# Performance work log

Hardware: AMD Instinct MI355X
Metric: run time of the kernel (lower is better)

## Reference

```python
import jax, jax.numpy as jnp
import numpy as np

B, S, D, E, K, NS = 4, 1024, 1024, 8, 2, 2
H = 4 * D
TEMP = 0.1
SCALE = 0.02


def setup_inputs() -> dict:
    key = jax.random.key(0)
    ks = jax.random.split(key, 12)
    f32 = jnp.float32
    return {
        "x": jax.random.normal(ks[0], (B, S, D), f32),
        "Ws1": jax.random.normal(ks[1], (NS, D, H), f32) * SCALE,
        "bs1": jnp.zeros((NS, H), f32),
        "Ws2": jax.random.normal(ks[2], (NS, H, D), f32) * SCALE,
        "bs2": jnp.zeros((NS, D), f32),
        "We1": jax.random.normal(ks[3], (E, D, H), f32) * SCALE,
        "be1": jnp.zeros((E, H), f32),
        "We2": jax.random.normal(ks[4], (E, H, D), f32) * SCALE,
        "be2": jnp.zeros((E, D), f32),
        "Wr": jax.random.normal(ks[5], (D, E), f32) * SCALE,
        "br": jnp.zeros((E,), f32),
        "gumbel": jax.random.gumbel(ks[6], (B, S, E), f32),
    }


def reference(x, Ws1, bs1, Ws2, bs2, We1, be1, We2, be2, Wr, br, gumbel):
    act = jax.nn.gelu
    # shared experts: dense FFN per shared expert, summed over experts
    hs = act(jnp.einsum('bsd,edh->ebsh', x, Ws1) + bs1[:, None, None, :])
    shared_sum = (jnp.einsum('ebsh,ehd->ebsd', hs, Ws2)
                  + bs2[:, None, None, :]).sum(axis=0)  # [B,S,D]
    # routing experts: ALL experts computed densely over all tokens
    he = act(jnp.einsum('bsd,edh->ebsh', x, We1) + be1[:, None, None, :])
    all_experts = jnp.einsum('ebsh,ehd->ebsd', he, We2) + be2[:, None, None, :]  # [E,B,S,D]
    # router + gumbel-softmax top-k selection
    logits = x @ Wr + br                                  # [B,S,E]
    router_probs = jax.nn.softmax((logits + gumbel) / TEMP, axis=-1)
    chosen = jax.lax.top_k(router_probs, K)[1]            # [B,S,K] int
    one_hot = jax.nn.one_hot(chosen, E, dtype=x.dtype)    # [B,S,K,E]
    # unweighted sum of selected experts' outputs (sum over k and experts)
    out = jnp.einsum('bske,ebsd->bsd', one_hot, all_experts)
    return out + shared_sum
```

## Files before the change

kernel.cpp:

```cpp
#include <hip/hip_runtime.h>
#include <cstdint>
#include <cstddef>

#define T_TOK 4096
#define DDIM 1024
#define HDIM 4096
#define NEXP 8
#define NSHARED 2
#define RT_CAP 9216

typedef unsigned short ushort_t;
typedef __attribute__((ext_vector_type(8))) short short8;
typedef __attribute__((ext_vector_type(4))) float f32x4;

__device__ inline ushort_t f2bf(float f) {
  unsigned u = __float_as_uint(f);
  u += 0x7fffu + ((u >> 16) & 1u);
  return (ushort_t)(u >> 16);
}

__device__ inline void async_copy16(const ushort_t* g, ushort_t* l) {
  __builtin_amdgcn_global_load_lds(
      (const __attribute__((address_space(1))) void*)g,
      (__attribute__((address_space(3))) void*)l, 16, 0, 0);
}

__device__ inline float gelu_tanh(float x) {
  float x2 = x * x;
  float t = fmaf(0.07135481627133721f, x2, 1.5957691216057308f);
  float e = __expf(-x * t);
  return x * __builtin_amdgcn_rcpf(1.0f + e);
}

__device__ inline void swizzle_xy(int* bx, int* by) {
  int l = blockIdx.x + gridDim.x * blockIdx.y;
  int g = l >> 8;
  *bx = (l & 7) + (g << 3);
  *by = (l >> 3) & 31;
}

#define PIPE_BOUNDARY()                                     \
  __builtin_amdgcn_sched_barrier(0);                        \
  asm volatile("s_waitcnt vmcnt(4)" ::: "memory");          \
  __builtin_amdgcn_s_barrier();                             \
  asm volatile("" ::: "memory");                            \
  __builtin_amdgcn_sched_barrier(0);

__global__ __launch_bounds__(256) void router_kernel(
    const float* __restrict__ x, const float* __restrict__ Wr,
    const float* __restrict__ br, const float* __restrict__ gum,
    int* __restrict__ choice, int* __restrict__ cnt) {
  int lane = threadIdx.x & 63;
  int wv = blockIdx.x * 4 + (threadIdx.x >> 6);
  if (wv >= T_TOK) return;
  const float* xr = x + (long)wv * DDIM;
  float acc[NEXP] = {0.f, 0.f, 0.f, 0.f, 0.f, 0.f, 0.f, 0.f};
  for (int d = lane; d < DDIM; d += 64) {
    float xv = xr[d];
    const float* w = Wr + d * NEXP;
#pragma unroll
    for (int e = 0; e < NEXP; e++) acc[e] += xv * w[e];
  }
#pragma unroll
  for (int e = 0; e < NEXP; e++) {
    float v = acc[e];
#pragma unroll
    for (int o = 32; o > 0; o >>= 1) v += __shfl_down(v, o);
    acc[e] = v;
  }
  if (lane == 0) {
    float vals[NEXP];
#pragma unroll
    for (int e = 0; e < NEXP; e++) vals[e] = acc[e] + br[e] + gum[(long)wv * NEXP + e];
    int i1 = 0; float b1 = vals[0];
#pragma unroll
    for (int e = 1; e < NEXP; e++) if (vals[e] > b1) { b1 = vals[e]; i1 = e; }
    int i2 = -1; float b2 = -3.4e38f;
#pragma unroll
    for (int e = 0; e < NEXP; e++) if (e != i1 && vals[e] > b2) { b2 = vals[e]; i2 = e; }
    choice[wv] = i1 | (i2 << 4);
    atomicAdd(&cnt[i1], 1);
    atomicAdd(&cnt[i2], 1);
  }
}

__global__ void prefix_kernel(const int* __restrict__ cnt, int* __restrict__ base,
                              int* __restrict__ fill) {
  if (threadIdx.x == 0 && blockIdx.x == 0) {
    int off = 0;
    for (int e = 0; e < NEXP; e++) {
      base[e] = off;
      off += (cnt[e] + 127) & ~127;
      fill[e] = 0;
    }
  }
}

__global__ __launch_bounds__(256) void scatter_kernel(
    const int* __restrict__ choice, const int* __restrict__ base,
    int* __restrict__ fill, int* __restrict__ idx, int* __restrict__ pos) {
  int t = blockIdx.x * 256 + threadIdx.x;
  if (t >= T_TOK) return;
  int c = choice[t];
  int e1 = c & 15, e2 = (c >> 4) & 15;
  int p1 = base[e1] + atomicAdd(&fill[e1], 1);
  idx[p1] = t; pos[2 * t] = p1;
  int p2 = base[e2] + atomicAdd(&fill[e2], 1);
  idx[p2] = t; pos[2 * t + 1] = p2;
}

__global__ __launch_bounds__(256) void cast_x_kernel(
    const float* __restrict__ in, ushort_t* __restrict__ out, int n4) {
  int i = blockIdx.x * 256 + threadIdx.x;
  if (i >= n4) return;
  float4 v = ((const float4*)in)[i];
  ushort4 o = make_ushort4(f2bf(v.x), f2bf(v.y), f2bf(v.z), f2bf(v.w));
  ((ushort4*)out)[i] = o;
}

__global__ __launch_bounds__(256) void transpose_cast10(
    const float* __restrict__ inS, const float* __restrict__ inE,
    ushort_t* __restrict__ out, int R, int C) {
  __shared__ float tile[32][33];
  int z = blockIdx.z;
  const float* in = (z < NSHARED) ? inS + (size_t)z * R * C
                                  : inE + (size_t)(z - NSHARED) * R * C;
  ushort_t* op = out + (size_t)z * R * C;
  int c0 = blockIdx.x * 32, r0 = blockIdx.y * 32;
  int tx = threadIdx.x, ty = threadIdx.y;
#pragma unroll
  for (int k = 0; k < 4; k++)
    tile[ty + 8 * k][tx] = in[(long)(r0 + ty + 8 * k) * C + (c0 + tx)];
  __syncthreads();
#pragma unroll
  for (int k = 0; k < 4; k++)
    op[(long)(c0 + ty + 8 * k) * R + (r0 + tx)] = f2bf(tile[tx][ty + 8 * k]);
}

__global__ __launch_bounds__(256) void gemm1_kernel(
    const ushort_t* __restrict__ xb, const ushort_t* __restrict__ W1t,
    const float* __restrict__ bs1, const float* __restrict__ be1,
    ushort_t* __restrict__ h_sh, ushort_t* __restrict__ h_rt,
    const int* __restrict__ cnt, const int* __restrict__ base,
    const int* __restrict__ idx) {
  __shared__ ushort_t As[3][4096];
  __shared__ ushort_t Bs[3][4096];

  int tid = threadIdx.x;
  int z = blockIdx.z;
  int bx, by; swizzle_xy(&bx, &by);
  int row0 = by * 128, col0 = bx * 128;
  bool sh = (z < NSHARED);

  int e = 0, M = T_TOK, base_e = 0;
  const ushort_t* Bp;
  const float* bias;
  if (sh) {
    Bp = W1t + (size_t)z * HDIM * DDIM;
    bias = bs1 + (size_t)z * HDIM;
  } else {
    e = z - NSHARED; M = cnt[e];
    if (row0 >= M) return;
    base_e = base[e];
    Bp = W1t + (size_t)(NSHARED + e) * HDIM * DDIM;
    bias = be1 + (size_t)e * HDIM;
  }

  int tq = tid & 3, tr = tid >> 2;
  const ushort_t *aP0, *aP1;
  if (sh) {
    aP0 = xb + (size_t)(row0 + tr) * DDIM + tq * 8;
    aP1 = aP0 + (size_t)64 * DDIM;
  } else {
    int s1 = row0 + tr;      if (s1 > M - 1) s1 = M - 1;
    int s2 = row0 + tr + 64; if (s2 > M - 1) s2 = M - 1;
    aP0 = xb + (size_t)idx[base_e + s1] * DDIM + tq * 8;
    aP1 = xb + (size_t)idx[base_e + s2] * DDIM + tq * 8;
  }
  const ushort_t* bP0 = Bp + (size_t)(col0 + tr) * DDIM + tq * 8;
  const ushort_t* bP1 = bP0 + (size_t)64 * DDIM;

  int lane = tid & 63, wv = tid >> 6;
  int wr = wv >> 1, wc = wv & 1;
  int ln = lane & 15, quad = lane >> 4;
  f32x4 acc[4][4] = {};
  const int ofsA = (wr * 64 + ln) * 32 + quad * 8;
  const int ofsB = (wc * 64 + ln) * 32 + quad * 8;

#define G1_STAGE(t, c)                                            \
  {                                                               \
    size_t kk = (size_t)(t) * 32;                                 \
    async_copy16(aP0 + kk, As[c] + tid * 8);                      \
    async_copy16(aP1 + kk, As[c] + tid * 8 + 2048);               \
    async_copy16(bP0 + kk, Bs[c] + tid * 8);                      \
    async_copy16(bP1 + kk, Bs[c] + tid * 8 + 2048);               \
  }

#define G1_COMPUTE(c)                                             \
  {                                                               \
    const ushort_t* aL = As[c] + ofsA;                            \
    const ushort_t* bL = Bs[c] + ofsB;                            \
    short8 af[4], bf[4];                                          \
    _Pragma("unroll") for (int i = 0; i < 4; i++) {               \
      af[i] = *(const short8*)(aL + i * 512);                     \
      bf[i] = *(const short8*)(bL + i * 512);                     \
    }                                                             \
    __builtin_amdgcn_s_setprio(1);                                \
    _Pragma("unroll") for (int i = 0; i < 4; i++)                 \
      _Pragma("unroll") for (int j = 0; j < 4; j++)               \
        acc[i][j] = __builtin_amdgcn_mfma_f32_16x16x32_bf16(      \
            af[i], bf[j], acc[i][j], 0, 0, 0);                    \
    __builtin_amdgcn_s_setprio(0);                                \
  }

  const int NT = DDIM / 32;
  G1_STAGE(0, 0);
  G1_STAGE(1, 1);
  PIPE_BOUNDARY();

  int c0 = 0, c1 = 1, c2 = 2;
  for (int t = 0; t < NT - 2; ++t) {
    G1_STAGE(t + 2, c2);
    G1_COMPUTE(c0);
    PIPE_BOUNDARY();
    int tmp = c0; c0 = c1; c1 = c2; c2 = tmp;
  }
  G1_COMPUTE(c0);
  __syncthreads();
  G1_COMPUTE(c1);

#pragma unroll
  for (int i = 0; i < 4; i++) {
    int rowB = row0 + wr * 64 + i * 16 + quad * 4;
#pragma unroll
    for (int j = 0; j < 4; j++) {
      int col = col0 + wc * 64 + j * 16 + ln;
      float b = bias[col];
#pragma unroll
      for (int r = 0; r < 4; r++) {
        int t = rowB + r;
        float v = gelu_tanh(acc[i][j][r] + b);
        if (sh) {
          h_sh[(size_t)t * (2 * HDIM) + (size_t)z * HDIM + col] = f2bf(v);
        } else if (t < M) {
          h_rt[((size_t)base_e + t) * HDIM + col] = f2bf(v);
        }
      }
    }
  }
#undef G1_STAGE
#undef G1_COMPUTE
}

__global__ __launch_bounds__(256) void gemm2_kernel(
    const ushort_t* __restrict__ h_sh, const ushort_t* __restrict__ h_rt,
    const ushort_t* __restrict__ W2t, float* __restrict__ outShA,
    float* __restrict__ outShB, float* __restrict__ outRt,
    const int* __restrict__ cnt, const int* __restrict__ base) {
  __shared__ ushort_t As[3][4096];
  __shared__ ushort_t Bs[3][4096];

  int tid = threadIdx.x;
  int z = blockIdx.z;
  int bx, by; swizzle_xy(&bx, &by);
  int row0 = by * 128, col0 = bx * 128;
  bool sh = (z < NSHARED);

  int e = 0, M = T_TOK, base_e = 0;
  const ushort_t* Ap;
  long lda;
  const ushort_t* Bp;
  float* outP;
  if (sh) {
    Ap = h_sh + (size_t)z * HDIM;
    lda = 2 * HDIM;
    Bp = W2t + (size_t)z * DDIM * HDIM;
    outP = (z == 0) ? outShA : outShB;
  } else {
    e = z - NSHARED; M = cnt[e];
    if (row0 >= M) return;
    base_e = base[e];
    Ap = h_rt + (size_t)base_e * HDIM;
    lda = HDIM;
    Bp = W2t + (size_t)(NSHARED + e) * DDIM * HDIM;
    outP = outRt + (size_t)base_e * DDIM;
  }

  int tq = tid & 3, tr = tid >> 2;
  const ushort_t* aP0 = Ap + (long)(row0 + tr) * lda + tq * 8;
  const ushort_t* aP1 = aP0 + 64L * lda;
  const ushort_t* bP0 = Bp + (size_t)(col0 + tr) * HDIM + tq * 8;
  const ushort_t* bP1 = bP0 + (size_t)64 * HDIM;

  int lane = tid & 63, wv = tid >> 6;
  int wr = wv >> 1, wc = wv & 1;
  int ln = lane & 15, quad = lane >> 4;
  f32x4 acc[4][4] = {};
  const int ofsA = (wr * 64 + ln) * 32 + quad * 8;
  const int ofsB = (wc * 64 + ln) * 32 + quad * 8;

#define G2_STAGE(t, c)                                            \
  {                                                               \
    size_t kk = (size_t)(t) * 32;                                 \
    async_copy16(aP0 + kk, As[c] + tid * 8);                      \
    async_copy16(aP1 + kk, As[c] + tid * 8 + 2048);               \
    async_copy16(bP0 + kk, Bs[c] + tid * 8);                      \
    async_copy16(bP1 + kk, Bs[c] + tid * 8 + 2048);               \
  }

#define G2_COMPUTE(c)                                             \
  {                                                               \
    const ushort_t* aL = As[c] + ofsA;                            \
    const ushort_t* bL = Bs[c] + ofsB;                            \
    short8 af[4], bf[4];                                          \
    _Pragma("unroll") for (int i = 0; i < 4; i++) {               \
      af[i] = *(const short8*)(aL + i * 512);                     \
      bf[i] = *(const short8*)(bL + i * 512);                     \
    }                                                             \
    __builtin_amdgcn_s_setprio(1);                                \
    _Pragma("unroll") for (int i = 0; i < 4; i++)                 \
      _Pragma("unroll") for (int j = 0; j < 4; j++)               \
        acc[i][j] = __builtin_amdgcn_mfma_f32_16x16x32_bf16(      \
            af[i], bf[j], acc[i][j], 0, 0, 0);                    \
    __builtin_amdgcn_s_setprio(0);                                \
  }

  const int NT = HDIM / 32;
  G2_STAGE(0, 0);
  G2_STAGE(1, 1);
  PIPE_BOUNDARY();

  int c0 = 0, c1 = 1, c2 = 2;
  for (int t = 0; t < NT - 2; ++t) {
    G2_STAGE(t + 2, c2);
    G2_COMPUTE(c0);
    PIPE_BOUNDARY();
    int tmp = c0; c0 = c1; c1 = c2; c2 = tmp;
  }
  G2_COMPUTE(c0);
  __syncthreads();
  G2_COMPUTE(c1);

#pragma unroll
  for (int i = 0; i < 4; i++) {
    int rowB = row0 + wr * 64 + i * 16 + quad * 4;
#pragma unroll
    for (int j = 0; j < 4; j++) {
      int col = col0 + wc * 64 + j * 16 + ln;
#pragma unroll
      for (int r = 0; r < 4; r++) {
        int t = rowB + r;
        if (sh || t < M) outP[(size_t)t * DDIM + col] = acc[i][j][r];
      }
    }
  }
#undef G2_STAGE
#undef G2_COMPUTE
}

__global__ __launch_bounds__(256) void combine_kernel(
    const float* __restrict__ shA, const float* __restrict__ shB,
    const float* __restrict__ rt, const float* __restrict__ bs2,
    const float* __restrict__ be2, const int* __restrict__ choice,
    const int* __restrict__ pos, float* __restrict__ out) {
  int i = blockIdx.x * 256 + threadIdx.x;
  int t = i >> 8;
  int d4 = i & 255;
  int c = choice[t];
  int e1 = c & 15, e2 = (c >> 4) & 15;
  long p1 = (long)pos[2 * t] * 256 + d4;
  long p2 = (long)pos[2 * t + 1] * 256 + d4;
  float4 a = ((const float4*)shA)[i];
  float4 b = ((const float4*)shB)[i];
  float4 r1 = ((const float4*)rt)[p1];
  float4 r2 = ((const float4*)rt)[p2];
  float4 b0 = ((const float4*)bs2)[d4];
  float4 b1 = ((const float4*)bs2)[256 + d4];
  float4 c1 = ((const float4*)be2)[e1 * 256 + d4];
  float4 c2 = ((const float4*)be2)[e2 * 256 + d4];
  float4 o;
  o.x = a.x + b.x + r1.x + r2.x + b0.x + b1.x + c1.x + c2.x;
  o.y = a.y + b.y + r1.y + r2.y + b0.y + b1.y + c1.y + c2.y;
  o.z = a.z + b.z + r1.z + r2.z + b0.z + b1.z + c1.z + c2.z;
  o.w = a.w + b.w + r1.w + r2.w + b0.w + b1.w + c1.w + c2.w;
  ((float4*)out)[i] = o;
}

extern "C" void kernel_launch(void* const* d_in, const int* in_sizes, int n_in,
                              void* d_out, int out_size, void* d_ws,
                              size_t ws_size, hipStream_t stream) {
  const float* x   = (const float*)d_in[0];
  const float* Ws1 = (const float*)d_in[1];
  const float* bs1 = (const float*)d_in[2];
  const float* Ws2 = (const float*)d_in[3];
  const float* bs2 = (const float*)d_in[4];
  const float* We1 = (const float*)d_in[5];
  const float* be1 = (const float*)d_in[6];
  const float* We2 = (const float*)d_in[7];
  const float* be2 = (const float*)d_in[8];
  const float* Wr  = (const float*)d_in[9];
  const float* br  = (const float*)d_in[10];
  const float* gum = (const float*)d_in[11];
  float* out = (float*)d_out;

  char* ws = (char*)d_ws;
  size_t off = 0;
  int* cnt    = (int*)(ws + off); off += 256;
  int* base   = (int*)(ws + off); off += 256;
  int* fill   = (int*)(ws + off); off += 256;
  int* choice = (int*)(ws + off); off += T_TOK * 4;
  int* idx    = (int*)(ws + off); off += RT_CAP * 4;
  int* pos    = (int*)(ws + off); off += T_TOK * 8;
  off = (off + 255) & ~(size_t)255;
  ushort_t* xb   = (ushort_t*)(ws + off); off += (size_t)T_TOK * DDIM * 2;
  ushort_t* W1t  = (ushort_t*)(ws + off); off += (size_t)10 * HDIM * DDIM * 2;
  ushort_t* W2t  = (ushort_t*)(ws + off); off += (size_t)10 * DDIM * HDIM * 2;
  ushort_t* h_sh = (ushort_t*)(ws + off); off += (size_t)T_TOK * 2 * HDIM * 2;
  ushort_t* h_rt = (ushort_t*)(ws + off); off += (size_t)RT_CAP * HDIM * 2;
  float* outShA = (float*)W1t;
  float* outShB = outShA + (size_t)T_TOK * DDIM;
  float* outRt  = outShB + (size_t)T_TOK * DDIM;
  (void)ws_size;

  hipMemsetAsync(cnt, 0, 256, stream);
  router_kernel<<<T_TOK / 4, 256, 0, stream>>>(x, Wr, br, gum, choice, cnt);
  prefix_kernel<<<1, 64, 0, stream>>>(cnt, base, fill);
  scatter_kernel<<<T_TOK / 256, 256, 0, stream>>>(choice, base, fill, idx, pos);
  cast_x_kernel<<<(T_TOK * DDIM / 4 + 255) / 256, 256, 0, stream>>>(
      x, xb, T_TOK * DDIM / 4);

  transpose_cast10<<<dim3(HDIM / 32, DDIM / 32, 10), dim3(32, 8), 0, stream>>>(
      Ws1, We1, W1t, DDIM, HDIM);
  transpose_cast10<<<dim3(DDIM / 32, HDIM / 32, 10), dim3(32, 8), 0, stream>>>(
      Ws2, We2, W2t, HDIM, DDIM);

  gemm1_kernel<<<dim3(HDIM / 128, T_TOK / 128, NSHARED + NEXP), 256, 0, stream>>>(
      xb, W1t, bs1, be1, h_sh, h_rt, cnt, base, idx);
  gemm2_kernel<<<dim3(DDIM / 128, T_TOK / 128, NSHARED + NEXP), 256, 0, stream>>>(
      h_sh, h_rt, W2t, outShA, outShB, outRt, cnt, base);
  combine_kernel<<<T_TOK * DDIM / 4 / 256, 256, 0, stream>>>(
      outShA, outShB, outRt, bs2, be2, choice, pos, out);

  (void)in_sizes; (void)n_in; (void)out_size;
}
```

Measured before the change: 1.111 ms.

## Enlarge GEMM tiles to 256x256 with 512-thread blocks and k-split LDS layout

Both expert GEMMs move from 128x128 tiles with 256 threads to 256x256 tiles with 512 threads (8 waves, each computing 128x64). The shared-memory layout changes so that each thread copies one row's two 16-element k-chunks into separate halves, and fragment reads follow that layout. The aim is higher arithmetic intensity per loaded byte and fewer blocks re-reading the same weights. In exchange it uses 96KB of LDS per block and more accumulator registers, and routed experts with small token counts now waste more of the larger row tiles.

```diff
diff --git a/kernel.cpp b/kernel.cpp
--- a/kernel.cpp
+++ b/kernel.cpp
@@ -30,13 +30,6 @@
   float t = fmaf(0.07135481627133721f, x2, 1.5957691216057308f);
   float e = __expf(-x * t);
   return x * __builtin_amdgcn_rcpf(1.0f + e);
-}
-
-__device__ inline void swizzle_xy(int* bx, int* by) {
-  int l = blockIdx.x + gridDim.x * blockIdx.y;
-  int g = l >> 8;
-  *bx = (l & 7) + (g << 3);
-  *by = (l >> 3) & 31;
 }
 
 #define PIPE_BOUNDARY()                                     \
@@ -137,25 +130,27 @@
     op[(long)(c0 + ty + 8 * k) * R + (r0 + tx)] = f2bf(tile[tx][ty + 8 * k]);
 }
 
-__global__ __launch_bounds__(256) void gemm1_kernel(
+__global__ __launch_bounds__(512, 2) void gemm1_kernel(
     const ushort_t* __restrict__ xb, const ushort_t* __restrict__ W1t,
     const float* __restrict__ bs1, const float* __restrict__ be1,
     ushort_t* __restrict__ h_sh, ushort_t* __restrict__ h_rt,
     const int* __restrict__ cnt, const int* __restrict__ base,
     const int* __restrict__ idx) {
-  __shared__ ushort_t As[3][4096];
-  __shared__ ushort_t Bs[3][4096];
+  __shared__ ushort_t As[3][8192];
+  __shared__ ushort_t Bs[3][8192];
 
   int tid = threadIdx.x;
   int z = blockIdx.z;
-  int bx, by; swizzle_xy(&bx, &by);
-  int row0 = by * 128, col0 = bx * 128;
-  bool sh = (z < NSHARED);
+  int l = blockIdx.x + gridDim.x * blockIdx.y;
+  int bx = (l & 7) + ((l >> 7) << 3);
+  int by = (l >> 3) & 15;
+  int row0 = by * 256, col0 = bx * 256;
+  bool shd = (z < NSHARED);
 
   int e = 0, M = T_TOK, base_e = 0;
   const ushort_t* Bp;
   const float* bias;
-  if (sh) {
+  if (shd) {
     Bp = W1t + (size_t)z * HDIM * DDIM;
     bias = bs1 + (size_t)z * HDIM;
   } else {
@@ -166,52 +161,43 @@
     bias = be1 + (size_t)e * HDIM;
   }
 
-  int tq = tid & 3, tr = tid >> 2;
-  const ushort_t *aP0, *aP1;
-  if (sh) {
-    aP0 = xb + (size_t)(row0 + tr) * DDIM + tq * 8;
-    aP1 = aP0 + (size_t)64 * DDIM;
+  int srow = tid & 255, sch = tid >> 8;
+  const ushort_t* aP;
+  if (shd) {
+    aP = xb + (size_t)(row0 + srow) * DDIM + sch * 8;
   } else {
-    int s1 = row0 + tr;      if (s1 > M - 1) s1 = M - 1;
-    int s2 = row0 + tr + 64; if (s2 > M - 1) s2 = M - 1;
-    aP0 = xb + (size_t)idx[base_e + s1] * DDIM + tq * 8;
-    aP1 = xb + (size_t)idx[base_e + s2] * DDIM + tq * 8;
-  }
-  const ushort_t* bP0 = Bp + (size_t)(col0 + tr) * DDIM + tq * 8;
-  const ushort_t* bP1 = bP0 + (size_t)64 * DDIM;
+    int s1 = row0 + srow; if (s1 > M - 1) s1 = M - 1;
+    aP = xb + (size_t)idx[base_e + s1] * DDIM + sch * 8;
+  }
+  const ushort_t* bP = Bp + (size_t)(col0 + srow) * DDIM + sch * 8;
 
   int lane = tid & 63, wv = tid >> 6;
-  int wr = wv >> 1, wc = wv & 1;
+  int wr = wv >> 2, wc = wv & 3;
   int ln = lane & 15, quad = lane >> 4;
-  f32x4 acc[4][4] = {};
-  const int ofsA = (wr * 64 + ln) * 32 + quad * 8;
-  const int ofsB = (wc * 64 + ln) * 32 + quad * 8;
-
-#define G1_STAGE(t, c)                                            \
-  {                                                               \
-    size_t kk = (size_t)(t) * 32;                                 \
-    async_copy16(aP0 + kk, As[c] + tid * 8);                      \
-    async_copy16(aP1 + kk, As[c] + tid * 8 + 2048);               \
-    async_copy16(bP0 + kk, Bs[c] + tid * 8);                      \
-    async_copy16(bP1 + kk, Bs[c] + tid * 8 + 2048);               \
-  }
-
-#define G1_COMPUTE(c)                                             \
-  {                                                               \
-    const ushort_t* aL = As[c] + ofsA;                            \
-    const ushort_t* bL = Bs[c] + ofsB;                            \
-    short8 af[4], bf[4];                                          \
-    _Pragma("unroll") for (int i = 0; i < 4; i++) {               \
-      af[i] = *(const short8*)(aL + i * 512);                     \
-      bf[i] = *(const short8*)(bL + i * 512);                     \
-    }                                                             \
-    __builtin_amdgcn_s_setprio(1);                                \
-    _Pragma("unroll") for (int i = 0; i < 4; i++)                 \
-      _Pragma("unroll") for (int j = 0; j < 4; j++)               \
-        acc[i][j] = __builtin_amdgcn_mfma_f32_16x16x32_bf16(      \
-            af[i], bf[j], acc[i][j], 0, 0, 0);                    \
-    __builtin_amdgcn_s_setprio(0);                                \
-  }
+  f32x4 acc[8][4] = {};
+  const int rdA = quad * 2048 + (wr * 128 + ln) * 8;
+  const int rdB = quad * 2048 + (wc * 64 + ln) * 8;
+
+#define G1_STAGE(t, c) { size_t kk = (size_t)(t) * 32;            \
+    async_copy16(aP + kk,      As[c] + tid * 8);                  \
+    async_copy16(aP + kk + 16, As[c] + tid * 8 + 4096);           \
+    async_copy16(bP + kk,      Bs[c] + tid * 8);                  \
+    async_copy16(bP + kk + 16, Bs[c] + tid * 8 + 4096); }
+
+#define G1_COMPUTE(c) {                                           \
+    const ushort_t* aB_ = As[c] + rdA;                            \
+    const ushort_t* bB_ = Bs[c] + rdB;                            \
+    short8 bfr[4];                                                \
+    _Pragma("unroll") for (int g = 0; g < 4; g++)                 \
+      bfr[g] = *(const short8*)(bB_ + g * 128);                   \
+    _Pragma("unroll") for (int f = 0; f < 8; f++) {               \
+      short8 afr = *(const short8*)(aB_ + f * 128);               \
+      __builtin_amdgcn_s_setprio(1);                              \
+      _Pragma("unroll") for (int g = 0; g < 4; g++)               \
+        acc[f][g] = __builtin_amdgcn_mfma_f32_16x16x32_bf16(      \
+            afr, bfr[g], acc[f][g], 0, 0, 0);                     \
+      __builtin_amdgcn_s_setprio(0);                              \
+    } }
 
   const int NT = DDIM / 32;
   G1_STAGE(0, 0);
@@ -230,17 +216,17 @@
   G1_COMPUTE(c1);
 
 #pragma unroll
-  for (int i = 0; i < 4; i++) {
-    int rowB = row0 + wr * 64 + i * 16 + quad * 4;
-#pragma unroll
-    for (int j = 0; j < 4; j++) {
-      int col = col0 + wc * 64 + j * 16 + ln;
+  for (int f = 0; f < 8; f++) {
+    int rowB = row0 + wr * 128 + f * 16 + quad * 4;
+#pragma unroll
+    for (int g = 0; g < 4; g++) {
+      int col = col0 + wc * 64 + g * 16 + ln;
       float b = bias[col];
 #pragma unroll
       for (int r = 0; r < 4; r++) {
         int t = rowB + r;
-        float v = gelu_tanh(acc[i][j][r] + b);
-        if (sh) {
+        float v = gelu_tanh(acc[f][g][r] + b);
+        if (shd) {
           h_sh[(size_t)t * (2 * HDIM) + (size_t)z * HDIM + col] = f2bf(v);
         } else if (t < M) {
           h_rt[((size_t)base_e + t) * HDIM + col] = f2bf(v);
@@ -252,26 +238,28 @@
 #undef G1_COMPUTE
 }
 
-__global__ __launch_bounds__(256) void gemm2_kernel(
+__global__ __launch_bounds__(512, 2) void gemm2_kernel(
     const ushort_t* __restrict__ h_sh, const ushort_t* __restrict__ h_rt,
     const ushort_t* __restrict__ W2t, float* __restrict__ outShA,
     float* __restrict__ outShB, float* __restrict__ outRt,
     const int* __restrict__ cnt, const int* __restrict__ base) {
-  __shared__ ushort_t As[3][4096];
-  __shared__ ushort_t Bs[3][4096];
+  __shared__ ushort_t As[3][8192];
+  __shared__ ushort_t Bs[3][8192];
 
   int tid = threadIdx.x;
   int z = blockIdx.z;
-  int bx, by; swizzle_xy(&bx, &by);
-  int row0 = by * 128, col0 = bx * 128;
-  bool sh = (z < NSHARED);
+  int l = blockIdx.x + gridDim.x * blockIdx.y;
+  int bx = l & 3;
+  int by = (l >> 2) & 15;
+  int row0 = by * 256, col0 = bx * 256;
+  bool shd = (z < NSHARED);
 
   int e = 0, M = T_TOK, base_e = 0;
   const ushort_t* Ap;
   long lda;
   const ushort_t* Bp;
   float* outP;
-  if (sh) {
+  if (shd) {
     Ap = h_sh + (size_t)z * HDIM;
     lda = 2 * HDIM;
     Bp = W2t + (size_t)z * DDIM * HDIM;
@@ -286,44 +274,39 @@
     outP = outRt + (size_t)base_e * DDIM;
   }
 
-  int tq = tid & 3, tr = tid >> 2;
-  const ushort_t* aP0 = Ap + (long)(row0 + tr) * lda + tq * 8;
-  const ushort_t* aP1 = aP0 + 64L * lda;
-  const ushort_t* bP0 = Bp + (size_t)(col0 + tr) * HDIM + tq * 8;
-  const ushort_t* bP1 = bP0 + (size_t)64 * HDIM;
+  int srow = tid & 255, sch = tid >> 8;
+  int s1 = row0 + srow;
+  if (!shd && s1 > M - 1) s1 = M - 1;
+  const ushort_t* aP = Ap + (long)s1 * lda + sch * 8;
+  const ushort_t* bP = Bp + (size_t)(col0 + srow) * HDIM + sch * 8;
 
   int lane = tid & 63, wv = tid >> 6;
-  int wr = wv >> 1, wc = wv & 1;
+  int wr = wv >> 2, wc = wv & 3;
   int ln = lane & 15, quad = lane >> 4;
-  f32x4 acc[4][4] = {};
-  const int ofsA = (wr * 64 + ln) * 32 + quad * 8;
-  const int ofsB = (wc * 64 + ln) * 32 + quad * 8;
-
-#define G2_STAGE(t, c)                                            \
-  {                                                               \
-    size_t kk = (size_t)(t) * 32;                                 \
-    async_copy16(aP0 + kk, As[c] + tid * 8);                      \
-    async_copy16(aP1 + kk, As[c] + tid * 8 + 2048);               \
-    async_copy16(bP0 + kk, Bs[c] + tid * 8);                      \
-    async_copy16(bP1 + kk, Bs[c] + tid * 8 + 2048);               \
-  }
-
-#define G2_COMPUTE(c)                                             \
-  {                                                               \
-    const ushort_t* aL = As[c] + ofsA;                            \
-    const ushort_t* bL = Bs[c] + ofsB;                            \
-    short8 af[4], bf[4];                                          \
-    _Pragma("unroll") for (int i = 0; i < 4; i++) {               \
-      af[i] = *(const short8*)(aL + i * 512);                     \
-      bf[i] = *(const short8*)(bL + i * 512);                     \
-    }                                                             \
-    __builtin_amdgcn_s_setprio(1);                                \
-    _Pragma("unroll") for (int i = 0; i < 4; i++)                 \
-      _Pragma("unroll") for (int j = 0; j < 4; j++)               \
-        acc[i][j] = __builtin_amdgcn_mfma_f32_16x16x32_bf16(      \
-            af[i], bf[j], acc[i][j], 0, 0, 0);                    \
-    __builtin_amdgcn_s_setprio(0);                                \
-  }
+  f32x4 acc[8][4] = {};
+  const int rdA = quad * 2048 + (wr * 128 + ln) * 8;
+  const int rdB = quad * 2048 + (wc * 64 + ln) * 8;
+
+#define G2_STAGE(t, c) { size_t kk = (size_t)(t) * 32;            \
+    async_copy16(aP + kk,      As[c] + tid * 8);                  \
+    async_copy16(aP + kk + 16, As[c] + tid * 8 + 4096);           \
+    async_copy16(bP + kk,      Bs[c] + tid * 8);                  \
+    async_copy16(bP + kk + 16, Bs[c] + tid * 8 + 4096); }
+
+#define G2_COMPUTE(c) {                                           \
+    const ushort_t* aB_ = As[c] + rdA;                            \
+    const ushort_t* bB_ = Bs[c] + rdB;                            \
+    short8 bfr[4];                                                \
+    _Pragma("unroll") for (int g = 0; g < 4; g++)                 \
+      bfr[g] = *(const short8*)(bB_ + g * 128);                   \
+    _Pragma("unroll") for (int f = 0; f < 8; f++) {               \
+      short8 afr = *(const short8*)(aB_ + f * 128);               \
+      __builtin_amdgcn_s_setprio(1);                              \
+      _Pragma("unroll") for (int g = 0; g < 4; g++)               \
+        acc[f][g] = __builtin_amdgcn_mfma_f32_16x16x32_bf16(      \
+            afr, bfr[g], acc[f][g], 0, 0, 0);                     \
+      __builtin_amdgcn_s_setprio(0);                              \
+    } }
 
   const int NT = HDIM / 32;
   G2_STAGE(0, 0);
@@ -342,15 +325,15 @@
   G2_COMPUTE(c1);
 
 #pragma unroll
-  for (int i = 0; i < 4; i++) {
-    int rowB = row0 + wr * 64 + i * 16 + quad * 4;
-#pragma unroll
-    for (int j = 0; j < 4; j++) {
-      int col = col0 + wc * 64 + j * 16 + ln;
+  for (int f = 0; f < 8; f++) {
+    int rowB = row0 + wr * 128 + f * 16 + quad * 4;
+#pragma unroll
+    for (int g = 0; g < 4; g++) {
+      int col = col0 + wc * 64 + g * 16 + ln;
 #pragma unroll
       for (int r = 0; r < 4; r++) {
         int t = rowB + r;
-        if (sh || t < M) outP[(size_t)t * DDIM + col] = acc[i][j][r];
+        if (shd || t < M) outP[(size_t)t * DDIM + col] = acc[f][g][r];
       }
     }
   }
@@ -434,9 +417,9 @@
   transpose_cast10<<<dim3(DDIM / 32, HDIM / 32, 10), dim3(32, 8), 0, stream>>>(
       Ws2, We2, W2t, HDIM, DDIM);
 
-  gemm1_kernel<<<dim3(HDIM / 128, T_TOK / 128, NSHARED + NEXP), 256, 0, stream>>>(
+  gemm1_kernel<<<dim3(16, 16, NSHARED + NEXP), 512, 0, stream>>>(
       xb, W1t, bs1, be1, h_sh, h_rt, cnt, base, idx);
-  gemm2_kernel<<<dim3(DDIM / 128, T_TOK / 128, NSHARED + NEXP), 256, 0, stream>>>(
+  gemm2_kernel<<<dim3(4, 16, NSHARED + NEXP), 512, 0, stream>>>(
       h_sh, h_rt, W2t, outShA, outShB, outRt, cnt, base);
   combine_kernel<<<T_TOK * DDIM / 4 / 256, 256, 0, stream>>>(
       outShA, outShB, outRt, bs2, be2, choice, pos, out);
```

Measured after the change: 1.390 ms. 25.1% more time.
